# Performance work log

Measured on AMD Instinct MI355X. Metric: run time of the kernel, lower is better.

Reference implementation:

```python
import jax, jax.numpy as jnp
import numpy as np

NEG_SLOPE = 0.2  # DGL GATConv default leaky_relu slope


def gat_conv(x, src, dst, W, attn_l, attn_r, bias, res_W):
    """DGL GATConv (eval mode, residual=True with linear res_fc, bias).
    x: [N, F_in]; src/dst: [E]; W: [F_in, H*D]; attn_l/r: [H, D];
    bias: [H*D]; res_W: [F_in, H*D]. Returns [N, H, D]."""
    N = x.shape[0]
    H, D = attn_l.shape
    feat = (x @ W).reshape(N, H, D)
    el = jnp.sum(feat * attn_l, axis=-1)  # [N, H]
    er = jnp.sum(feat * attn_r, axis=-1)  # [N, H]
    e = jax.nn.leaky_relu(el[src] + er[dst], NEG_SLOPE)  # [E, H]
    # edge softmax over incoming edges of each dst node (numerically stable)
    m = jnp.full((N, H), -jnp.inf, dtype=e.dtype).at[dst].max(e)
    ex = jnp.exp(e - m[dst])
    s = jnp.zeros((N, H), dtype=e.dtype).at[dst].add(ex)
    alpha = ex / s[dst]  # [E, H]
    # scatter-aggregate messages alpha * feat[src] into dst
    rst = jnp.zeros((N, H, D), dtype=x.dtype).at[dst].add(alpha[:, :, None] * feat[src])
    rst = rst + (x @ res_W).reshape(N, H, D) + bias.reshape(1, H, D)
    return rst


def setup_inputs() -> dict:
    key = jax.random.key(0)
    N, E, F_IN, HID, OUT, H = 20000, 320000, 128, 128, 128, 4
    ks = jax.random.split(key, 32)
    ki = iter(range(32))

    def rn(shape, scale=0.05):
        return jax.random.normal(ks[next(ki)], shape, dtype=jnp.float32) * scale

    inp = {
        "n_feat": jax.random.normal(ks[next(ki)], (N, F_IN), dtype=jnp.float32),
        "src": jax.random.randint(ks[next(ki)], (E,), 0, N, dtype=jnp.int32),
        "dst": jax.random.randint(ks[next(ki)], (E,), 0, N, dtype=jnp.int32),
        # input GATConv: F_IN -> H x HID
        "W0": rn((F_IN, H * HID)), "al0": rn((H, HID)), "ar0": rn((H, HID)),
        "b0": rn((H * HID,)), "rW0": rn((F_IN, H * HID)),
        "DW0": rn((H * HID, HID)), "Db0": rn((HID,)),
        # middle GATConv: HID -> H x HID
        "W1": rn((HID, H * HID)), "al1": rn((H, HID)), "ar1": rn((H, HID)),
        "b1": rn((H * HID,)), "rW1": rn((HID, H * HID)),
        "DW1": rn((H * HID, HID)), "Db1": rn((HID,)),
        # output GATConv: HID -> H x OUT
        "W2": rn((HID, H * OUT)), "al2": rn((H, OUT)), "ar2": rn((H, OUT)),
        "b2": rn((H * OUT,)), "rW2": rn((HID, H * OUT)),
    }
    return inp


def reference(n_feat, src, dst,
              W0, al0, ar0, b0, rW0, DW0, Db0,
              W1, al1, ar1, b1, rW1, DW1, Db1,
              W2, al2, ar2, b2, rW2):
    N = n_feat.shape[0]
    relu = jax.nn.relu
    # input GAT block
    h = relu(gat_conv(n_feat, src, dst, W0, al0, ar0, b0, rW0))  # [N, H, HID]
    h = relu(h.reshape(N, -1) @ DW0 + Db0)                        # [N, HID]
    # middle GAT block
    h = relu(gat_conv(h, src, dst, W1, al1, ar1, b1, rW1))
    h = relu(h.reshape(N, -1) @ DW1 + Db1)
    # output GAT + head-mean + graph max pooling (single graph)
    h = relu(gat_conv(h, src, dst, W2, al2, ar2, b2, rW2))        # [N, H, OUT]
    h = relu(jnp.mean(h, axis=-2))                                 # [N, OUT]
    return jnp.max(h, axis=0, keepdims=True)                       # [1, OUT]
```

## Files before the change

### kernel.cpp

```cpp
#include <hip/hip_runtime.h>
#include <hip/hip_bf16.h>


typedef __attribute__((ext_vector_type(8))) short bf16x8;
typedef __attribute__((ext_vector_type(4))) float f32x4;
typedef __hip_bfloat16 bf16_t;

__device__ __forceinline__ unsigned int pack_bf16(float lo, float hi) {
  return (((unsigned int)__bfloat16_as_ushort(__float2bfloat16(hi))) << 16) |
         (unsigned int)__bfloat16_as_ushort(__float2bfloat16(lo));
}

__device__ __forceinline__ void gload_lds16(const void* g, void* l) {
  __builtin_amdgcn_global_load_lds(
      (const __attribute__((address_space(1))) void*)g,
      (__attribute__((address_space(3))) void*)l, 16, 0, 0);
}

__global__ __launch_bounds__(256) void prep_weights(
    const float* __restrict__ W0, const float* __restrict__ rW0,
    const float* __restrict__ W1, const float* __restrict__ rW1,
    const float* __restrict__ W2, const float* __restrict__ rW2,
    const float* __restrict__ DW0, const float* __restrict__ DW1,
    bf16_t* __restrict__ out) {
  int idx = blockIdx.x * 256 + threadIdx.x;
  float v;
  if (idx < 393216) {
    int mat = idx / 131072;
    int off = idx & 131071;
    int n = off >> 7, k = off & 127;
    const float* W = (mat == 0) ? W0 : (mat == 1) ? W1 : W2;
    const float* rW = (mat == 0) ? rW0 : (mat == 1) ? rW1 : rW2;
    v = (n < 512) ? W[k * 512 + n] : rW[k * 512 + (n - 512)];
  } else {
    int rem = idx - 393216;
    int mat = rem >> 16;
    int off = rem & 65535;
    int n = off >> 9, k = off & 511;
    const float* DW = mat ? DW1 : DW0;
    v = DW[k * 128 + n];
  }
  out[idx] = __float2bfloat16(v);
}

__global__ __launch_bounds__(256) void alr_kernel(
    const float* __restrict__ W0, const float* __restrict__ W1,
    const float* __restrict__ W2, const float* __restrict__ al0,
    const float* __restrict__ ar0, const float* __restrict__ al1,
    const float* __restrict__ ar1, const float* __restrict__ al2,
    const float* __restrict__ ar2, float* __restrict__ ALR) {
  int idx = blockIdx.x * 256 + threadIdx.x;
  if (idx >= 3 * 128 * 8) return;
  int L = idx >> 10;
  int k = (idx >> 3) & 127;
  int c = idx & 7;
  int h = c & 3;
  const float* W = (L == 0) ? W0 : (L == 1) ? W1 : W2;
  const float* a = (c < 4) ? ((L == 0) ? al0 : (L == 1) ? al1 : al2)
                           : ((L == 0) ? ar0 : (L == 1) ? ar1 : ar2);
  float s = 0.f;
  for (int d = 0; d < 128; d++) s += W[k * 512 + h * 128 + d] * a[h * 128 + d];
  ALR[idx] = s;
}

__global__ __launch_bounds__(256) void convert_bf16(const float* __restrict__ in,
                                                    bf16_t* __restrict__ out, int n) {
  int i = (blockIdx.x * 256 + threadIdx.x) * 4;
  if (i < n) {
    float4 v = *(const float4*)(in + i);
    out[i + 0] = __float2bfloat16(v.x);
    out[i + 1] = __float2bfloat16(v.y);
    out[i + 2] = __float2bfloat16(v.z);
    out[i + 3] = __float2bfloat16(v.w);
  }
}

__global__ __launch_bounds__(256) void mfma_gemm128(
    const bf16_t* __restrict__ A, const bf16_t* __restrict__ Bt,
    bf16_t* __restrict__ C, int M, int ldc, int K) {
  __shared__ bf16_t As[128 * 64];
  __shared__ bf16_t Bs[128 * 64];
  int tid = threadIdx.x;
  int lane = tid & 63, wave = tid >> 6;
  int q = lane >> 4, r16 = lane & 15;
  int wm = (wave >> 1) * 64, wn = (wave & 1) * 64;
  int rowBase = blockIdx.y * 128, colBase = blockIdx.x * 128;

  f32x4 acc[4][4] = {};

  for (int k0 = 0; k0 < K; k0 += 64) {
#pragma unroll
    for (int p = 0; p < 4; p++) {
      int slotb = (wave * 4 + p) * 64;
      int s = slotb + lane;
      int r = s >> 3;
      int c = (s & 7) ^ (r & 7);
      int gr = rowBase + r;
      if (gr > M - 1) gr = M - 1;
      gload_lds16(A + (size_t)gr * K + k0 + c * 8, (char*)As + (size_t)slotb * 16);
      gload_lds16(Bt + (size_t)(colBase + r) * K + k0 + c * 8,
                  (char*)Bs + (size_t)slotb * 16);
    }
    __syncthreads();
#pragma unroll
    for (int ks = 0; ks < 64; ks += 32) {
      int koff = ks >> 3;
      bf16x8 af[4], bfr[4];
#pragma unroll
      for (int i = 0; i < 4; i++) {
        int R = wm + i * 16 + r16;
        int slot = R * 8 + ((q + koff) ^ (R & 7));
        af[i] = *(const bf16x8*)((const char*)As + (size_t)slot * 16);
      }
#pragma unroll
      for (int j = 0; j < 4; j++) {
        int R = wn + j * 16 + r16;
        int slot = R * 8 + ((q + koff) ^ (R & 7));
        bfr[j] = *(const bf16x8*)((const char*)Bs + (size_t)slot * 16);
      }
#pragma unroll
      for (int i = 0; i < 4; i++)
#pragma unroll
        for (int j = 0; j < 4; j++)
          acc[i][j] = __builtin_amdgcn_mfma_f32_16x16x32_bf16(af[i], bfr[j], acc[i][j], 0, 0, 0);
    }
    __syncthreads();
  }

  int odd = lane & 1;
  int colb0 = r16 & ~1;
#pragma unroll
  for (int i = 0; i < 4; i++) {
#pragma unroll
    for (int r = 0; r < 4; r++) {
      int row = rowBase + wm + i * 16 + q * 4 + r;
#pragma unroll
      for (int jp = 0; jp < 2; jp++) {
        float a0 = acc[i][2 * jp][r];
        float a1 = acc[i][2 * jp + 1][r];
        float p0 = __shfl_xor(a0, 1);
        float p1 = __shfl_xor(a1, 1);
        float lo = odd ? p1 : a0;
        float hi = odd ? a1 : p0;
        int col = colBase + wn + (2 * jp + odd) * 16 + colb0;
        if (row < M)
          *(unsigned int*)(C + (size_t)row * ldc + col) = pack_bf16(lo, hi);
      }
    }
  }
}

__global__ __launch_bounds__(256) void mfma_gemm64(
    const bf16_t* __restrict__ A, const bf16_t* __restrict__ Bt,
    const float* __restrict__ bias, bf16_t* __restrict__ C,
    int M, int ldc, int K) {
  __shared__ bf16_t As[64 * 64];
  __shared__ bf16_t Bs[64 * 64];
  int tid = threadIdx.x;
  int lane = tid & 63, wave = tid >> 6;
  int q = lane >> 4, r16 = lane & 15;
  int wm = (wave >> 1) * 32, wn = (wave & 1) * 32;
  int rowBase = blockIdx.y * 64, colBase = blockIdx.x * 64;

  f32x4 acc[2][2] = {};

  for (int k0 = 0; k0 < K; k0 += 64) {
#pragma unroll
    for (int p = 0; p < 2; p++) {
      int slotb = (wave * 2 + p) * 64;
      int s = slotb + lane;
      int r = s >> 3;
      int c = (s & 7) ^ (r & 7);
      int gr = rowBase + r;
      if (gr > M - 1) gr = M - 1;
      gload_lds16(A + (size_t)gr * K + k0 + c * 8, (char*)As + (size_t)slotb * 16);
      gload_lds16(Bt + (size_t)(colBase + r) * K + k0 + c * 8,
                  (char*)Bs + (size_t)slotb * 16);
    }
    __syncthreads();
#pragma unroll
    for (int ks = 0; ks < 64; ks += 32) {
      int koff = ks >> 3;
      bf16x8 af[2], bfr[2];
#pragma unroll
      for (int i = 0; i < 2; i++) {
        int R = wm + i * 16 + r16;
        int slot = R * 8 + ((q + koff) ^ (R & 7));
        af[i] = *(const bf16x8*)((const char*)As + (size_t)slot * 16);
      }
#pragma unroll
      for (int j = 0; j < 2; j++) {
        int R = wn + j * 16 + r16;
        int slot = R * 8 + ((q + koff) ^ (R & 7));
        bfr[j] = *(const bf16x8*)((const char*)Bs + (size_t)slot * 16);
      }
#pragma unroll
      for (int i = 0; i < 2; i++)
#pragma unroll
        for (int j = 0; j < 2; j++)
          acc[i][j] = __builtin_amdgcn_mfma_f32_16x16x32_bf16(af[i], bfr[j], acc[i][j], 0, 0, 0);
    }
    __syncthreads();
  }

  int odd = lane & 1;
  int colb0 = r16 & ~1;
#pragma unroll
  for (int i = 0; i < 2; i++) {
#pragma unroll
    for (int r = 0; r < 4; r++) {
      int row = rowBase + wm + i * 16 + q * 4 + r;
      float a0 = acc[i][0][r];
      float a1 = acc[i][1][r];
      float p0 = __shfl_xor(a0, 1);
      float p1 = __shfl_xor(a1, 1);
      float lo = odd ? p1 : a0;
      float hi = odd ? a1 : p0;
      int col = colBase + wn + odd * 16 + colb0;
      if (row < M) {
        float o0 = fmaxf(lo + bias[col], 0.f);
        float o1 = fmaxf(hi + bias[col + 1], 0.f);
        *(unsigned int*)(C + (size_t)row * ldc + col) = pack_bf16(o0, o1);
      }
    }
  }
}

__global__ __launch_bounds__(256) void el_er_fast(
    const bf16_t* __restrict__ x, const float* __restrict__ ALR,
    float* __restrict__ el, float* __restrict__ er, int N) {
  int wave = threadIdx.x >> 6, l = threadIdx.x & 63;
  int n = blockIdx.x * 4 + wave;
  if (n >= N) return;
  unsigned int xp = *(const unsigned int*)(x + (size_t)n * 128 + 2 * l);
  float f0 = __uint_as_float(xp << 16);
  float f1 = __uint_as_float(xp & 0xffff0000u);
  const float* A0 = ALR + (size_t)(2 * l) * 8;
  float s[8];
#pragma unroll
  for (int c = 0; c < 8; c++) s[c] = f0 * A0[c] + f1 * A0[8 + c];
#pragma unroll
  for (int off = 32; off; off >>= 1)
#pragma unroll
    for (int c = 0; c < 8; c++) s[c] += __shfl_xor(s[c], off);
  if (l == 0) {
#pragma unroll
    for (int h = 0; h < 4; h++) {
      el[n * 4 + h] = s[h];
      er[n * 4 + h] = s[4 + h];
    }
  }
}

__global__ __launch_bounds__(256) void count_kernel(const int* __restrict__ dst,
                                                    int* __restrict__ counts, int E) {
  int i = blockIdx.x * blockDim.x + threadIdx.x;
  if (i < E) atomicAdd(&counts[dst[i]], 1);
}

__global__ __launch_bounds__(1024) void scan_kernel(const int* __restrict__ counts,
                                                    int* __restrict__ row_ptr,
                                                    int* __restrict__ cursor, int N) {
  __shared__ int sums[1024];
  int t = threadIdx.x;
  int chunk = (N + 1023) / 1024;
  int begin = t * chunk;
  int end = begin + chunk;
  if (end > N) end = N;
  int s = 0;
  for (int i = begin; i < end; i++) s += counts[i];
  sums[t] = s;
  __syncthreads();
  for (int off = 1; off < 1024; off <<= 1) {
    int v = (t >= off) ? sums[t - off] : 0;
    __syncthreads();
    sums[t] += v;
    __syncthreads();
  }
  int run = (t == 0) ? 0 : sums[t - 1];
  for (int i = begin; i < end; i++) {
    row_ptr[i] = run;
    cursor[i] = run;
    run += counts[i];
  }
  if (t == 1023) row_ptr[N] = sums[1023];
}

__global__ __launch_bounds__(256) void scatter_kernel(
    const int* __restrict__ src, const int* __restrict__ dst,
    int* __restrict__ cursor, int* __restrict__ edge_src, int E) {
  int i = blockIdx.x * blockDim.x + threadIdx.x;
  if (i < E) {
    int d = dst[i];
    int pos = atomicAdd(&cursor[d], 1);
    edge_src[pos] = src[i];
  }
}

__global__ __launch_bounds__(256) void gat_agg_kernel(
    const bf16_t* __restrict__ fused,
    const float* __restrict__ el, const float* __restrict__ er,
    const float* __restrict__ bias, const int* __restrict__ row_ptr,
    const int* __restrict__ edge_src, bf16_t* __restrict__ out, int N) {
  int n = blockIdx.x;
  int h = threadIdx.x >> 6;
  int l = threadIdx.x & 63;
  int g = l >> 4, t = l & 15;
  int start = row_ptr[n];
  int deg = row_ptr[n + 1] - start;
  float er_nh = er[n * 4 + h];

  float m = -3.402823466e38f;
  for (int i = l; i < deg; i += 64) {
    int s = edge_src[start + i];
    float e = el[s * 4 + h] + er_nh;
    e = (e > 0.f) ? e : 0.2f * e;
    m = fmaxf(m, e);
  }
#pragma unroll
  for (int off = 32; off; off >>= 1) m = fmaxf(m, __shfl_xor(m, off));

  float acc[8] = {};
  float ssum = 0.f;
  for (int i = g; i < deg; i += 4) {
    int s = edge_src[start + i];
    float e = el[s * 4 + h] + er_nh;
    e = (e > 0.f) ? e : 0.2f * e;
    float w = __expf(e - m);
    ssum += w;
    uint4 fp = *(const uint4*)(fused + (size_t)s * 1024 + h * 128 + t * 8);
    unsigned int u0 = fp.x, u1 = fp.y, u2 = fp.z, u3 = fp.w;
    acc[0] += w * __uint_as_float(u0 << 16);
    acc[1] += w * __uint_as_float(u0 & 0xffff0000u);
    acc[2] += w * __uint_as_float(u1 << 16);
    acc[3] += w * __uint_as_float(u1 & 0xffff0000u);
    acc[4] += w * __uint_as_float(u2 << 16);
    acc[5] += w * __uint_as_float(u2 & 0xffff0000u);
    acc[6] += w * __uint_as_float(u3 << 16);
    acc[7] += w * __uint_as_float(u3 & 0xffff0000u);
  }
#pragma unroll
  for (int off = 16; off <= 32; off <<= 1) {
    ssum += __shfl_xor(ssum, off);
#pragma unroll
    for (int d = 0; d < 8; d++) acc[d] += __shfl_xor(acc[d], off);
  }

  if (g == 0) {
    float inv = (deg > 0) ? 1.f / ssum : 0.f;
    uint4 rp = *(const uint4*)(fused + (size_t)n * 1024 + 512 + h * 128 + t * 8);
    const float* bp = bias + h * 128 + t * 8;
    unsigned int ru[4] = {rp.x, rp.y, rp.z, rp.w};
    unsigned int ow[4];
#pragma unroll
    for (int j = 0; j < 4; j++) {
      float o0 = fmaxf(acc[2 * j] * inv + __uint_as_float(ru[j] << 16) + bp[2 * j], 0.f);
      float o1 = fmaxf(acc[2 * j + 1] * inv + __uint_as_float(ru[j] & 0xffff0000u) + bp[2 * j + 1], 0.f);
      ow[j] = pack_bf16(o0, o1);
    }
    *(uint4*)(out + (size_t)n * 512 + h * 128 + t * 8) = make_uint4(ow[0], ow[1], ow[2], ow[3]);
  }
}

__global__ __launch_bounds__(128) void pool_kernel(const bf16_t* __restrict__ g,
                                                   float* __restrict__ out, int N) {
  int d = threadIdx.x;
  float mx = 0.f;
  for (int n = blockIdx.x; n < N; n += gridDim.x) {
    const bf16_t* p = g + (size_t)n * 512 + d;
    float v = 0.25f * (__bfloat162float(p[0]) + __bfloat162float(p[128]) +
                       __bfloat162float(p[256]) + __bfloat162float(p[384]));
    mx = fmaxf(mx, v);
  }
  atomicMax((int*)out + d, __float_as_int(mx));
}

extern "C" void kernel_launch(void* const* d_in, const int* in_sizes, int n_in,
                              void* d_out, int out_size, void* d_ws, size_t ws_size,
                              hipStream_t stream) {
  const float* n_feat = (const float*)d_in[0];
  const int* src = (const int*)d_in[1];
  const int* dst = (const int*)d_in[2];
  const float* W0 = (const float*)d_in[3];
  const float* al0 = (const float*)d_in[4];
  const float* ar0 = (const float*)d_in[5];
  const float* b0 = (const float*)d_in[6];
  const float* rW0 = (const float*)d_in[7];
  const float* DW0 = (const float*)d_in[8];
  const float* Db0 = (const float*)d_in[9];
  const float* W1 = (const float*)d_in[10];
  const float* al1 = (const float*)d_in[11];
  const float* ar1 = (const float*)d_in[12];
  const float* b1 = (const float*)d_in[13];
  const float* rW1 = (const float*)d_in[14];
  const float* DW1 = (const float*)d_in[15];
  const float* Db1 = (const float*)d_in[16];
  const float* W2 = (const float*)d_in[17];
  const float* al2 = (const float*)d_in[18];
  const float* ar2 = (const float*)d_in[19];
  const float* b2 = (const float*)d_in[20];
  const float* rW2 = (const float*)d_in[21];

  const int N = in_sizes[0] / 128;
  const int E = in_sizes[1];

  bf16_t* xbf = (bf16_t*)d_ws;
  bf16_t* fusedFR = xbf + (size_t)N * 128;
  bf16_t* outC = fusedFR + (size_t)N * 1024;
  bf16_t* denseD = outC + (size_t)N * 512;
  bf16_t* wts = denseD + (size_t)N * 128;
  float* ALR = (float*)(wts + 524288);
  float* el = ALR + 3072;
  float* er = el + (size_t)N * 4;
  int* counts = (int*)(er + (size_t)N * 4);
  int* row_ptr = counts + N;
  int* cursor = row_ptr + (N + 1);
  int* edge_src = cursor + N;

  bf16_t* FW0 = wts;
  bf16_t* FW1 = wts + 131072;
  bf16_t* FW2 = wts + 262144;
  bf16_t* DWt0 = wts + 393216;
  bf16_t* DWt1 = wts + 458752;

  prep_weights<<<2048, 256, 0, stream>>>(W0, rW0, W1, rW1, W2, rW2, DW0, DW1, wts);
  alr_kernel<<<12, 256, 0, stream>>>(W0, W1, W2, al0, ar0, al1, ar1, al2, ar2, ALR);
  convert_bf16<<<(N * 128 / 4 + 255) / 256, 256, 0, stream>>>(n_feat, xbf, N * 128);

  hipMemsetAsync(counts, 0, (size_t)N * sizeof(int), stream);
  count_kernel<<<(E + 255) / 256, 256, 0, stream>>>(dst, counts, E);
  scan_kernel<<<1, 1024, 0, stream>>>(counts, row_ptr, cursor, N);
  scatter_kernel<<<(E + 255) / 256, 256, 0, stream>>>(src, dst, cursor, edge_src, E);

  dim3 gF(8, (N + 127) / 128);
  dim3 gD(2, (N + 63) / 64);
  int gEL = (N + 3) / 4;

  mfma_gemm128<<<gF, 256, 0, stream>>>(xbf, FW0, fusedFR, N, 1024, 128);
  el_er_fast<<<gEL, 256, 0, stream>>>(xbf, ALR, el, er, N);
  gat_agg_kernel<<<N, 256, 0, stream>>>(fusedFR, el, er, b0, row_ptr, edge_src, outC, N);
  mfma_gemm64<<<gD, 256, 0, stream>>>(outC, DWt0, Db0, denseD, N, 128, 512);

  mfma_gemm128<<<gF, 256, 0, stream>>>(denseD, FW1, fusedFR, N, 1024, 128);
  el_er_fast<<<gEL, 256, 0, stream>>>(denseD, ALR + 1024, el, er, N);
  gat_agg_kernel<<<N, 256, 0, stream>>>(fusedFR, el, er, b1, row_ptr, edge_src, outC, N);
  mfma_gemm64<<<gD, 256, 0, stream>>>(outC, DWt1, Db1, denseD, N, 128, 512);

  mfma_gemm128<<<gF, 256, 0, stream>>>(denseD, FW2, fusedFR, N, 1024, 128);
  el_er_fast<<<gEL, 256, 0, stream>>>(denseD, ALR + 2048, el, er, N);
  gat_agg_kernel<<<N, 256, 0, stream>>>(fusedFR, el, er, b2, row_ptr, edge_src, outC, N);

  hipMemsetAsync(d_out, 0, 128 * sizeof(float), stream);
  pool_kernel<<<256, 128, 0, stream>>>(outC, (float*)d_out, N);
}
```

Before: 506.8 us.

## Fuse prep kernels into one launch and fold el/er into GEMM grid

Merges the weight transpose/convert, attention-vector projection, input bf16 conversion and the two memsets into a single multi-role kernel. The weight transpose now goes through a shared-memory tile, so both its reads and writes are coalesced. The per-layer el/er computation becomes an extra column of blocks in the feature GEMM grid, which removes three launches. This cuts launch overhead and per-kernel tail effects. In exchange the prep kernel and the GEMM have more branching, and the el/er blocks run serial per-thread dot products.

```diff
diff --git a/kernel.cpp b/kernel.cpp
--- a/kernel.cpp
+++ b/kernel.cpp
@@ -17,74 +17,125 @@
       (__attribute__((address_space(3))) void*)l, 16, 0, 0);
 }
 
-__global__ __launch_bounds__(256) void prep_weights(
+__global__ __launch_bounds__(256) void mega_prep(
     const float* __restrict__ W0, const float* __restrict__ rW0,
     const float* __restrict__ W1, const float* __restrict__ rW1,
     const float* __restrict__ W2, const float* __restrict__ rW2,
     const float* __restrict__ DW0, const float* __restrict__ DW1,
-    bf16_t* __restrict__ out) {
-  int idx = blockIdx.x * 256 + threadIdx.x;
-  float v;
-  if (idx < 393216) {
-    int mat = idx / 131072;
-    int off = idx & 131071;
-    int n = off >> 7, k = off & 127;
-    const float* W = (mat == 0) ? W0 : (mat == 1) ? W1 : W2;
-    const float* rW = (mat == 0) ? rW0 : (mat == 1) ? rW1 : rW2;
-    v = (n < 512) ? W[k * 512 + n] : rW[k * 512 + (n - 512)];
+    const float* __restrict__ al0, const float* __restrict__ ar0,
+    const float* __restrict__ al1, const float* __restrict__ ar1,
+    const float* __restrict__ al2, const float* __restrict__ ar2,
+    const float* __restrict__ n_feat, bf16_t* __restrict__ wts,
+    float* __restrict__ ALR, bf16_t* __restrict__ xbf,
+    int* __restrict__ counts, float* __restrict__ d_out_f, int N) {
+  __shared__ float tile[32][33];
+  int b = blockIdx.x, tid = threadIdx.x;
+  int r = tid >> 5, c = tid & 31;
+
+  if (b < 384) {
+    int mat = b >> 6;
+    int t = b & 63;
+    int kt = t >> 4, nt = t & 15;
+    int L = mat >> 1, isR = mat & 1;
+    const float* S = (L == 0) ? (isR ? rW0 : W0)
+                   : (L == 1) ? (isR ? rW1 : W1) : (isR ? rW2 : W2);
+    bf16_t* D = wts + L * 131072 + isR * 65536;
+#pragma unroll
+    for (int rr = 0; rr < 4; rr++)
+      tile[r + rr * 8][c] = S[(kt * 32 + r + rr * 8) * 512 + nt * 32 + c];
+    __syncthreads();
+#pragma unroll
+    for (int rr = 0; rr < 4; rr++)
+      D[(nt * 32 + r + rr * 8) * 128 + kt * 32 + c] =
+          __float2bfloat16(tile[c][r + rr * 8]);
+  } else if (b < 512) {
+    int i = b - 384;
+    int mat = i >> 6;
+    int t = i & 63;
+    int kt = t & 15, nt = t >> 4;
+    const float* S = mat ? DW1 : DW0;
+    bf16_t* D = wts + 393216 + mat * 65536;
+#pragma unroll
+    for (int rr = 0; rr < 4; rr++)
+      tile[r + rr * 8][c] = S[(kt * 32 + r + rr * 8) * 128 + nt * 32 + c];
+    __syncthreads();
+#pragma unroll
+    for (int rr = 0; rr < 4; rr++)
+      D[(nt * 32 + r + rr * 8) * 512 + kt * 32 + c] =
+          __float2bfloat16(tile[c][r + rr * 8]);
+  } else if (b < 524) {
+    int idx = (b - 512) * 256 + tid;
+    if (idx < 3072) {
+      int L = idx >> 10;
+      int k = (idx >> 3) & 127;
+      int cc = idx & 7;
+      int h = cc & 3;
+      const float* W = (L == 0) ? W0 : (L == 1) ? W1 : W2;
+      const float* a = (cc < 4) ? ((L == 0) ? al0 : (L == 1) ? al1 : al2)
+                                : ((L == 0) ? ar0 : (L == 1) ? ar1 : ar2);
+      float s = 0.f;
+      for (int d = 0; d < 128; d++) s += W[k * 512 + h * 128 + d] * a[h * 128 + d];
+      ALR[idx] = s;
+    }
+  } else if (b < 3024) {
+    int i = ((b - 524) * 256 + tid) * 4;
+    if (i < N * 128) {
+      float4 v = *(const float4*)(n_feat + i);
+      xbf[i + 0] = __float2bfloat16(v.x);
+      xbf[i + 1] = __float2bfloat16(v.y);
+      xbf[i + 2] = __float2bfloat16(v.z);
+      xbf[i + 3] = __float2bfloat16(v.w);
+    }
   } else {
-    int rem = idx - 393216;
-    int mat = rem >> 16;
-    int off = rem & 65535;
-    int n = off >> 9, k = off & 511;
-    const float* DW = mat ? DW1 : DW0;
-    v = DW[k * 128 + n];
-  }
-  out[idx] = __float2bfloat16(v);
-}
-
-__global__ __launch_bounds__(256) void alr_kernel(
-    const float* __restrict__ W0, const float* __restrict__ W1,
-    const float* __restrict__ W2, const float* __restrict__ al0,
-    const float* __restrict__ ar0, const float* __restrict__ al1,
-    const float* __restrict__ ar1, const float* __restrict__ al2,
-    const float* __restrict__ ar2, float* __restrict__ ALR) {
-  int idx = blockIdx.x * 256 + threadIdx.x;
-  if (idx >= 3 * 128 * 8) return;
-  int L = idx >> 10;
-  int k = (idx >> 3) & 127;
-  int c = idx & 7;
-  int h = c & 3;
-  const float* W = (L == 0) ? W0 : (L == 1) ? W1 : W2;
-  const float* a = (c < 4) ? ((L == 0) ? al0 : (L == 1) ? al1 : al2)
-                           : ((L == 0) ? ar0 : (L == 1) ? ar1 : ar2);
-  float s = 0.f;
-  for (int d = 0; d < 128; d++) s += W[k * 512 + h * 128 + d] * a[h * 128 + d];
-  ALR[idx] = s;
-}
-
-__global__ __launch_bounds__(256) void convert_bf16(const float* __restrict__ in,
-                                                    bf16_t* __restrict__ out, int n) {
-  int i = (blockIdx.x * 256 + threadIdx.x) * 4;
-  if (i < n) {
-    float4 v = *(const float4*)(in + i);
-    out[i + 0] = __float2bfloat16(v.x);
-    out[i + 1] = __float2bfloat16(v.y);
-    out[i + 2] = __float2bfloat16(v.z);
-    out[i + 3] = __float2bfloat16(v.w);
-  }
-}
-
-__global__ __launch_bounds__(256) void mfma_gemm128(
+    for (int i = tid; i < N; i += 256) counts[i] = 0;
+    if (tid < 128) d_out_f[tid] = 0.f;
+  }
+}
+
+__global__ __launch_bounds__(256) void gemm128el(
     const bf16_t* __restrict__ A, const bf16_t* __restrict__ Bt,
-    bf16_t* __restrict__ C, int M, int ldc, int K) {
+    const float* __restrict__ ALRl, bf16_t* __restrict__ C,
+    float* __restrict__ el, float* __restrict__ er, int M, int ldc, int K) {
   __shared__ bf16_t As[128 * 64];
   __shared__ bf16_t Bs[128 * 64];
   int tid = threadIdx.x;
+  int rowBase = blockIdx.y * 128;
+
+  if (blockIdx.x == 8) {
+    float* sALR = (float*)As;
+#pragma unroll
+    for (int j = 0; j < 4; j++) sALR[tid * 4 + j] = ALRl[tid * 4 + j];
+    __syncthreads();
+    int row = rowBase + (tid >> 1);
+    int half = tid & 1;
+    if (row < M) {
+      const bf16_t* xr = A + (size_t)row * K + half * 64;
+      float s[8] = {};
+#pragma unroll
+      for (int g = 0; g < 8; g++) {
+        bf16x8 v = *(const bf16x8*)(xr + g * 8);
+#pragma unroll
+        for (int e = 0; e < 8; e++) {
+          float f = __uint_as_float(((unsigned int)(unsigned short)v[e]) << 16);
+          const float* Ak = sALR + (half * 64 + g * 8 + e) * 8;
+#pragma unroll
+          for (int cc = 0; cc < 8; cc++) s[cc] += f * Ak[cc];
+        }
+      }
+#pragma unroll
+      for (int cc = 0; cc < 8; cc++) s[cc] += __shfl_xor(s[cc], 1);
+      if (half == 0)
+        *(float4*)(el + row * 4) = make_float4(s[0], s[1], s[2], s[3]);
+      else
+        *(float4*)(er + row * 4) = make_float4(s[4], s[5], s[6], s[7]);
+    }
+    return;
+  }
+
   int lane = tid & 63, wave = tid >> 6;
   int q = lane >> 4, r16 = lane & 15;
   int wm = (wave >> 1) * 64, wn = (wave & 1) * 64;
-  int rowBase = blockIdx.y * 128, colBase = blockIdx.x * 128;
+  int colBase = blockIdx.x * 128;
 
   f32x4 acc[4][4] = {};
 
@@ -222,32 +273,6 @@
         float o1 = fmaxf(hi + bias[col + 1], 0.f);
         *(unsigned int*)(C + (size_t)row * ldc + col) = pack_bf16(o0, o1);
       }
-    }
-  }
-}
-
-__global__ __launch_bounds__(256) void el_er_fast(
-    const bf16_t* __restrict__ x, const float* __restrict__ ALR,
-    float* __restrict__ el, float* __restrict__ er, int N) {
-  int wave = threadIdx.x >> 6, l = threadIdx.x & 63;
-  int n = blockIdx.x * 4 + wave;
-  if (n >= N) return;
-  unsigned int xp = *(const unsigned int*)(x + (size_t)n * 128 + 2 * l);
-  float f0 = __uint_as_float(xp << 16);
-  float f1 = __uint_as_float(xp & 0xffff0000u);
-  const float* A0 = ALR + (size_t)(2 * l) * 8;
-  float s[8];
-#pragma unroll
-  for (int c = 0; c < 8; c++) s[c] = f0 * A0[c] + f1 * A0[8 + c];
-#pragma unroll
-  for (int off = 32; off; off >>= 1)
-#pragma unroll
-    for (int c = 0; c < 8; c++) s[c] += __shfl_xor(s[c], off);
-  if (l == 0) {
-#pragma unroll
-    for (int h = 0; h < 4; h++) {
-      el[n * 4 + h] = s[h];
-      er[n * 4 + h] = s[4 + h];
     }
   }
 }
@@ -423,33 +448,28 @@
   bf16_t* DWt0 = wts + 393216;
   bf16_t* DWt1 = wts + 458752;
 
-  prep_weights<<<2048, 256, 0, stream>>>(W0, rW0, W1, rW1, W2, rW2, DW0, DW1, wts);
-  alr_kernel<<<12, 256, 0, stream>>>(W0, W1, W2, al0, ar0, al1, ar1, al2, ar2, ALR);
-  convert_bf16<<<(N * 128 / 4 + 255) / 256, 256, 0, stream>>>(n_feat, xbf, N * 128);
-
-  hipMemsetAsync(counts, 0, (size_t)N * sizeof(int), stream);
+  mega_prep<<<3025, 256, 0, stream>>>(
+      W0, rW0, W1, rW1, W2, rW2, DW0, DW1,
+      al0, ar0, al1, ar1, al2, ar2,
+      n_feat, wts, ALR, xbf, counts, (float*)d_out, N);
+
   count_kernel<<<(E + 255) / 256, 256, 0, stream>>>(dst, counts, E);
   scan_kernel<<<1, 1024, 0, stream>>>(counts, row_ptr, cursor, N);
   scatter_kernel<<<(E + 255) / 256, 256, 0, stream>>>(src, dst, cursor, edge_src, E);
 
-  dim3 gF(8, (N + 127) / 128);
+  dim3 gF(9, (N + 127) / 128);
   dim3 gD(2, (N + 63) / 64);
-  int gEL = (N + 3) / 4;
-
-  mfma_gemm128<<<gF, 256, 0, stream>>>(xbf, FW0, fusedFR, N, 1024, 128);
-  el_er_fast<<<gEL, 256, 0, stream>>>(xbf, ALR, el, er, N);
+
+  gemm128el<<<gF, 256, 0, stream>>>(xbf, FW0, ALR, fusedFR, el, er, N, 1024, 128);
   gat_agg_kernel<<<N, 256, 0, stream>>>(fusedFR, el, er, b0, row_ptr, edge_src, outC, N);
   mfma_gemm64<<<gD, 256, 0, stream>>>(outC, DWt0, Db0, denseD, N, 128, 512);
 
-  mfma_gemm128<<<gF, 256, 0, stream>>>(denseD, FW1, fusedFR, N, 1024, 128);
-  el_er_fast<<<gEL, 256, 0, stream>>>(denseD, ALR + 1024, el, er, N);
+  gemm128el<<<gF, 256, 0, stream>>>(denseD, FW1, ALR + 1024, fusedFR, el, er, N, 1024, 128);
   gat_agg_kernel<<<N, 256, 0, stream>>>(fusedFR, el, er, b1, row_ptr, edge_src, outC, N);
   mfma_gemm64<<<gD, 256, 0, stream>>>(outC, DWt1, Db1, denseD, N, 128, 512);
 
-  mfma_gemm128<<<gF, 256, 0, stream>>>(denseD, FW2, fusedFR, N, 1024, 128);
-  el_er_fast<<<gEL, 256, 0, stream>>>(denseD, ALR + 2048, el, er, N);
+  gemm128el<<<gF, 256, 0, stream>>>(denseD, FW2, ALR + 2048, fusedFR, el, er, N, 1024, 128);
   gat_agg_kernel<<<N, 256, 0, stream>>>(fusedFR, el, er, b2, row_ptr, edge_src, outC, N);
 
-  hipMemsetAsync(d_out, 0, 128 * sizeof(float), stream);
   pool_kernel<<<256, 128, 0, stream>>>(outC, (float*)d_out, N);
 }
```

Result: faster. 474.4 us (-6.4%).
